# Optimization experiments

Hardware: AMD Instinct MI355X
Metric: run time of the kernel (lower is better)

## Reference

```python
import jax, jax.numpy as jnp
import numpy as np

LORA_RANK = 16
LORA_ALPHA = 32.0
LORA_SCALE = LORA_ALPHA / LORA_RANK
W_BITS = 8
A_BITS = 8


def fake_quant(x, bits):
    """Symmetric per-tensor fake quantization with straight-through estimator."""
    qmax = 2.0 ** (bits - 1) - 1.0
    scale = jnp.maximum(jnp.max(jnp.abs(x)), 1e-8) / qmax
    q = jnp.clip(jnp.round(x / scale), -qmax, qmax) * scale
    return x + jax.lax.stop_gradient(q - x)  # STE


def quant_linear_lora(x, W, b, A, B):
    # x: [..., in], W: [out, in], A: [r, in], B: [out, r]
    xq = fake_quant(x, A_BITS)
    Wq = fake_quant(W, W_BITS)
    base = jnp.einsum('bsi,oi->bso', xq, Wq) + b
    lora = jnp.einsum('bsr,or->bso', jnp.einsum('bsi,ri->bsr', x, A), B)
    return base + LORA_SCALE * lora


def setup_inputs() -> dict:
    key = jax.random.key(0)
    ks = jax.random.split(key, 9)
    n_embd, d_ff, B_, S = 1024, 4096, 4, 2048
    s_in = 1.0 / np.sqrt(n_embd)
    s_ff = 1.0 / np.sqrt(d_ff)
    return {
        'hidden_states': jax.random.normal(ks[0], (B_, S, n_embd), jnp.float32),
        'W_fc': jax.random.normal(ks[1], (d_ff, n_embd), jnp.float32) * s_in,
        'b_fc': jax.random.normal(ks[2], (d_ff,), jnp.float32) * 0.02,
        'A_fc': jax.random.normal(ks[3], (LORA_RANK, n_embd), jnp.float32) * s_in,
        'B_fc': jax.random.normal(ks[4], (d_ff, LORA_RANK), jnp.float32) * 0.01,
        'W_proj': jax.random.normal(ks[5], (n_embd, d_ff), jnp.float32) * s_ff,
        'b_proj': jax.random.normal(ks[6], (n_embd,), jnp.float32) * 0.02,
        'A_proj': jax.random.normal(ks[7], (LORA_RANK, d_ff), jnp.float32) * s_ff,
        'B_proj': jax.random.normal(ks[8], (n_embd, LORA_RANK), jnp.float32) * 0.01,
    }


def reference(hidden_states, W_fc, b_fc, A_fc, B_fc, W_proj, b_proj, A_proj, B_proj):
    h = quant_linear_lora(hidden_states, W_fc, b_fc, A_fc, B_fc)
    h = jax.nn.gelu(h, approximate=False)  # nn.GELU() default = exact erf GELU
    h = quant_linear_lora(h, W_proj, b_proj, A_proj, B_proj)
    return h
```

## Files before the change

kernel.cpp:

```cpp
#include <hip/hip_runtime.h>
#include <stdint.h>

using i32x4 = __attribute__((ext_vector_type(4))) int;
using f32x4 = __attribute__((ext_vector_type(4))) float;
using f16x4 = __attribute__((ext_vector_type(4))) _Float16;

#define M_TOK 8192
#define N_EMB 1024
#define D_FF  4096

__device__ __forceinline__ void async_lds16(void* lds, const void* g) {
  __builtin_amdgcn_global_load_lds(
      (const __attribute__((address_space(1))) void*)g,
      (__attribute__((address_space(3))) void*)lds, 16, 0, 0);
}

__global__ void zero_slots_k(unsigned* s) {
  if (threadIdx.x < 16) s[threadIdx.x] = 0u;
}

__global__ void absmax_k(const float* __restrict__ p, long n, unsigned* __restrict__ slot) {
  long i = ((long)blockIdx.x * blockDim.x + threadIdx.x) * 4;
  long stride = (long)gridDim.x * blockDim.x * 4;
  float m = 0.f;
  for (; i < n; i += stride) {
    float4 v = *(const float4*)(p + i);
    m = fmaxf(m, fmaxf(fmaxf(fabsf(v.x), fabsf(v.y)), fmaxf(fabsf(v.z), fabsf(v.w))));
  }
  for (int o = 32; o; o >>= 1) m = fmaxf(m, __shfl_xor(m, o));
  __shared__ float sm[4];
  if ((threadIdx.x & 63) == 0) sm[threadIdx.x >> 6] = m;
  __syncthreads();
  if (threadIdx.x == 0) {
    m = fmaxf(fmaxf(sm[0], sm[1]), fmaxf(sm[2], sm[3]));
    atomicMax(slot, __float_as_uint(m));
  }
}

__global__ void quant_k(const float* __restrict__ p, int8_t* __restrict__ q, long n,
                        const unsigned* __restrict__ slot) {
  float inv = 127.f / fmaxf(__uint_as_float(*slot), 1e-8f);
  long i = ((long)blockIdx.x * blockDim.x + threadIdx.x) * 4;
  long stride = (long)gridDim.x * blockDim.x * 4;
  for (; i < n; i += stride) {
    float4 v = *(const float4*)(p + i);
    int b0 = (int)fminf(fmaxf(rintf(v.x * inv), -127.f), 127.f);
    int b1 = (int)fminf(fmaxf(rintf(v.y * inv), -127.f), 127.f);
    int b2 = (int)fminf(fmaxf(rintf(v.z * inv), -127.f), 127.f);
    int b3 = (int)fminf(fmaxf(rintf(v.w * inv), -127.f), 127.f);
    int w = (b0 & 0xff) | ((b1 & 0xff) << 8) | ((b2 & 0xff) << 16) | ((b3 & 0xff) << 24);
    *(int*)(q + i) = w;
  }
}

__global__ void prep_bfrag_k(const float* __restrict__ A, _Float16* __restrict__ Bp, int K) {
  int s = blockIdx.x;
  int l = threadIdx.x;
  int r = l & 15, g = l >> 4;
  float4 v = *(const float4*)(A + (long)r * K + s * 16 + g * 4);
  f16x4 h;
  h[0] = (_Float16)v.x; h[1] = (_Float16)v.y; h[2] = (_Float16)v.z; h[3] = (_Float16)v.w;
  *(f16x4*)(Bp + ((long)s * 64 + l) * 4) = h;
}

__global__ __launch_bounds__(512) void lora_quant_k(
    const float* __restrict__ X, const _Float16* __restrict__ Bpre,
    const unsigned* __restrict__ slot, int8_t* __restrict__ Q,
    float* __restrict__ T, int K) {
  int lane = threadIdx.x & 63, wave = threadIdx.x >> 6;
  int row0 = blockIdx.x * 16;
  int r = lane & 15, g = lane >> 4;
  float inv = 127.f / fmaxf(__uint_as_float(*slot), 1e-8f);

  int kPerWave = K >> 3;
  int kbase = wave * kPerWave;
  const float* xrow = X + (long)(row0 + r) * K;
  int8_t* qrow = Q + (long)(row0 + r) * K;

  f32x4 acc = {0.f, 0.f, 0.f, 0.f};
  int nsteps = kPerWave >> 4;
#pragma unroll 4
  for (int s = 0; s < nsteps; s++) {
    int k = kbase + s * 16 + g * 4;
    float4 v = *(const float4*)(xrow + k);
    int b0 = (int)fminf(fmaxf(rintf(v.x * inv), -127.f), 127.f);
    int b1 = (int)fminf(fmaxf(rintf(v.y * inv), -127.f), 127.f);
    int b2 = (int)fminf(fmaxf(rintf(v.z * inv), -127.f), 127.f);
    int b3 = (int)fminf(fmaxf(rintf(v.w * inv), -127.f), 127.f);
    *(int*)(qrow + k) = (b0 & 0xff) | ((b1 & 0xff) << 8) | ((b2 & 0xff) << 16) | ((b3 & 0xff) << 24);
    f16x4 a;
    a[0] = (_Float16)v.x; a[1] = (_Float16)v.y; a[2] = (_Float16)v.z; a[3] = (_Float16)v.w;
    int gs = (kbase + s * 16) >> 4;
    f16x4 b = *(const f16x4*)(Bpre + ((long)gs * 64 + lane) * 4);
    acc = __builtin_amdgcn_mfma_f32_16x16x16f16(a, b, acc, 0, 0, 0);
  }

  __shared__ float part[8][16][17];
#pragma unroll
  for (int j = 0; j < 4; j++) part[wave][g * 4 + j][r] = acc[j];
  __syncthreads();
  int t = threadIdx.x;
  if (t < 256) {
    int m = t >> 4, rr = t & 15;
    float sum = 0.f;
#pragma unroll
    for (int w = 0; w < 8; w++) sum += part[w][m][rr];
    T[(long)(row0 + m) * 16 + rr] = 2.0f * sum;
  }
}

template <bool GELU, int NF>
__global__ __launch_bounds__(512, 2) void gemm8p(
    const int8_t* __restrict__ Aq, const int8_t* __restrict__ Bq,
    int N, int K,
    const unsigned* __restrict__ sa, const unsigned* __restrict__ sb,
    const float* __restrict__ bias,
    const float* __restrict__ T,
    const float* __restrict__ Bl,
    float* __restrict__ C, unsigned* hmax) {
  constexpr int BN = NF * 64;
  constexpr int BBUF = BN * 128;
  __shared__ __align__(16) int8_t lds[65536 + 2 * BBUF];
  int8_t* ldsA = lds;
  int8_t* ldsB = lds + 65536;

  int nwg = gridDim.x * gridDim.y;
  int lid = blockIdx.y * gridDim.x + blockIdx.x;
  int cpx = nwg >> 3;
  int nid = (lid & 7) * cpx + (lid >> 3);
  int bn = (nid % gridDim.x) * BN;
  int bm = (nid / gridDim.x) * 256;

  int t = threadIdx.x;
  int lane = t & 63, wave = t >> 6;
  int wr = wave >> 2, wc = wave & 3;
  int l16 = lane & 15, lq = lane >> 4;

  const int8_t* gA = Aq + (long)bm * K;
  const int8_t* gB = Bq + (long)bn * K;

  int aDst[4], aSrc[4];
#pragma unroll
  for (int i = 0; i < 4; i++) {
    int s = i * 512 + t, row = s >> 3;
    aDst[i] = s * 16;
    aSrc[i] = row * K + (((s & 7) ^ (row & 7)) << 4);
  }
  int bDst[NF], bSrc[NF];
#pragma unroll
  for (int i = 0; i < NF; i++) {
    int s = i * 512 + t, row = s >> 3;
    bDst[i] = s * 16;
    bSrc[i] = row * K + (((s & 7) ^ (row & 7)) << 4);
  }

  int aoff[8], boff[NF];
#pragma unroll
  for (int mf = 0; mf < 8; mf++) {
    int row = wr * 128 + mf * 16 + l16;
    aoff[mf] = row * 128 + ((lq ^ (row & 7)) << 4);
  }
#pragma unroll
  for (int nf = 0; nf < NF; nf++) {
    int row = wc * (NF * 16) + nf * 16 + l16;
    boff[nf] = row * 128 + ((lq ^ (row & 7)) << 4);
  }

  i32x4 acc[8][NF] = {};
  int KT = K >> 7;

#pragma unroll
  for (int i = 0; i < 4; i++) async_lds16(ldsA + aDst[i], gA + aSrc[i]);
#pragma unroll
  for (int i = 0; i < NF; i++) async_lds16(ldsB + bDst[i], gB + bSrc[i]);
#pragma unroll
  for (int i = 0; i < 4; i++) async_lds16(ldsA + 32768 + aDst[i], gA + aSrc[i] + 128);
  asm volatile("s_waitcnt vmcnt(4)" ::: "memory");
  __builtin_amdgcn_s_barrier();
  __builtin_amdgcn_sched_barrier(0);

  for (int kt = 0; kt < KT; ++kt) {
    const int8_t* Ab = ldsA + (kt & 1) * 32768;
    const int8_t* Bb = ldsB + (kt & 1) * BBUF;

    if (kt + 1 < KT) {
      long ko = (long)(kt + 1) * 128;
      int nb = ((kt + 1) & 1) * BBUF;
#pragma unroll
      for (int i = 0; i < NF; i++) async_lds16(ldsB + nb + bDst[i], gB + bSrc[i] + ko);
    }

#pragma unroll
    for (int ks = 0; ks < 2; ks++) {
      int kx = ks << 6;
      i32x4 av[8], bv[NF];
#pragma unroll
      for (int mf = 0; mf < 8; mf++) av[mf] = *(const i32x4*)(Ab + (aoff[mf] ^ kx));
#pragma unroll
      for (int nf = 0; nf < NF; nf++) bv[nf] = *(const i32x4*)(Bb + (boff[nf] ^ kx));
      __builtin_amdgcn_s_setprio(1);
#pragma unroll
      for (int mf = 0; mf < 8; mf++)
#pragma unroll
        for (int nf = 0; nf < NF; nf++)
          acc[mf][nf] = __builtin_amdgcn_mfma_i32_16x16x64_i8(av[mf], bv[nf], acc[mf][nf], 0, 0, 0);
      __builtin_amdgcn_s_setprio(0);
    }

    __builtin_amdgcn_sched_barrier(0);
    __builtin_amdgcn_s_barrier();
    if (kt + 2 < KT) {
      long ko = (long)(kt + 2) * 128;
      int nb = (kt & 1) * 32768;
#pragma unroll
      for (int i = 0; i < 4; i++) async_lds16(ldsA + nb + aDst[i], gA + aSrc[i] + ko);
      asm volatile("s_waitcnt vmcnt(4)" ::: "memory");
      __builtin_amdgcn_s_barrier();
      __builtin_amdgcn_sched_barrier(0);
    } else if (kt + 1 < KT) {
      asm volatile("s_waitcnt vmcnt(0)" ::: "memory");
      __builtin_amdgcn_s_barrier();
      __builtin_amdgcn_sched_barrier(0);
    }
  }

  float s = (fmaxf(__uint_as_float(*sa), 1e-8f) * (1.f / 127.f)) *
            (fmaxf(__uint_as_float(*sb), 1e-8f) * (1.f / 127.f));

  f16x4 af[8], bf[NF];
#pragma unroll
  for (int mf = 0; mf < 8; mf++) {
    int m = bm + wr * 128 + mf * 16 + l16;
    float4 tv = *(const float4*)(T + (long)m * 16 + lq * 4);
    f16x4 v; v[0] = (_Float16)tv.x; v[1] = (_Float16)tv.y; v[2] = (_Float16)tv.z; v[3] = (_Float16)tv.w;
    af[mf] = v;
  }
#pragma unroll
  for (int nf = 0; nf < NF; nf++) {
    int n = bn + wc * (NF * 16) + nf * 16 + l16;
    float4 bv4 = *(const float4*)(Bl + (long)n * 16 + lq * 4);
    f16x4 v; v[0] = (_Float16)bv4.x; v[1] = (_Float16)bv4.y; v[2] = (_Float16)bv4.z; v[3] = (_Float16)bv4.w;
    bf[nf] = v;
  }
  float bias_v[NF];
#pragma unroll
  for (int nf = 0; nf < NF; nf++) bias_v[nf] = bias[bn + wc * (NF * 16) + nf * 16 + l16];

  float lmax = 0.f;
#pragma unroll
  for (int mf = 0; mf < 8; mf++) {
#pragma unroll
    for (int nf = 0; nf < NF; nf++) {
      f32x4 fa = __builtin_amdgcn_mfma_f32_16x16x16f16(af[mf], bf[nf], f32x4{0.f, 0.f, 0.f, 0.f}, 0, 0, 0);
      int n = bn + wc * (NF * 16) + nf * 16 + l16;
#pragma unroll
      for (int j = 0; j < 4; j++) {
        int m = bm + wr * 128 + mf * 16 + lq * 4 + j;
        float v = s * (float)acc[mf][nf][j] + bias_v[nf] + fa[j];
        if constexpr (GELU) {
          v = 0.5f * v * (1.0f + erff(v * 0.70710678118654752f));
          lmax = fmaxf(lmax, fabsf(v));
        }
        C[(long)m * N + n] = v;
      }
    }
  }
  if constexpr (GELU) {
    for (int o = 32; o; o >>= 1) lmax = fmaxf(lmax, __shfl_xor(lmax, o));
    if (lane == 0) atomicMax(hmax, __float_as_uint(lmax));
  }
}

extern "C" void kernel_launch(void* const* d_in, const int* in_sizes, int n_in,
                              void* d_out, int out_size, void* d_ws, size_t ws_size,
                              hipStream_t stream) {
  const float* x   = (const float*)d_in[0];
  const float* Wfc = (const float*)d_in[1];
  const float* bfc = (const float*)d_in[2];
  const float* Afc = (const float*)d_in[3];
  const float* Bfc = (const float*)d_in[4];
  const float* Wpj = (const float*)d_in[5];
  const float* bpj = (const float*)d_in[6];
  const float* Apj = (const float*)d_in[7];
  const float* Bpj = (const float*)d_in[8];
  float* out = (float*)d_out;

  char* ws = (char*)d_ws;
  unsigned* slots = (unsigned*)ws;
  int8_t* qx  = (int8_t*)(ws + 256);
  int8_t* qwf = qx  + (size_t)M_TOK * N_EMB;
  int8_t* qwp = qwf + (size_t)D_FF * N_EMB;
  int8_t* qh  = qwp + (size_t)N_EMB * D_FF;
  float*  t1  = (float*)(qh + (size_t)M_TOK * D_FF);
  float*  t2  = t1  + (size_t)M_TOK * 16;
  _Float16* Bp1 = (_Float16*)(t2 + (size_t)M_TOK * 16);
  _Float16* Bp2 = Bp1 + (size_t)N_EMB * 16;
  float*  h   = (float*)(Bp2 + (size_t)D_FF * 16);

  zero_slots_k<<<1, 64, 0, stream>>>(slots);
  absmax_k<<<1024, 256, 0, stream>>>(x,   (long)M_TOK * N_EMB, slots + 0);
  absmax_k<<<1024, 256, 0, stream>>>(Wfc, (long)D_FF * N_EMB,  slots + 1);
  absmax_k<<<1024, 256, 0, stream>>>(Wpj, (long)N_EMB * D_FF,  slots + 2);

  quant_k<<<2048, 256, 0, stream>>>(Wfc, qwf, (long)D_FF * N_EMB, slots + 1);
  quant_k<<<2048, 256, 0, stream>>>(Wpj, qwp, (long)N_EMB * D_FF, slots + 2);

  prep_bfrag_k<<<N_EMB / 16, 64, 0, stream>>>(Afc, Bp1, N_EMB);
  prep_bfrag_k<<<D_FF / 16, 64, 0, stream>>>(Apj, Bp2, D_FF);

  lora_quant_k<<<M_TOK / 16, 512, 0, stream>>>(x, Bp1, slots + 0, qx, t1, N_EMB);

  gemm8p<true, 4><<<dim3(D_FF / 256, M_TOK / 256), 512, 0, stream>>>(
      qx, qwf, D_FF, N_EMB, slots + 0, slots + 1, bfc, t1, Bfc, h, slots + 3);

  lora_quant_k<<<M_TOK / 16, 512, 0, stream>>>(h, Bp2, slots + 3, qh, t2, D_FF);

  gemm8p<false, 2><<<dim3(N_EMB / 128, M_TOK / 256), 512, 0, stream>>>(
      qh, qwp, N_EMB, D_FF, slots + 3, slots + 2, bpj, t2, Bpj, out, nullptr);
}
```

Baseline: 280.2 us.

## Rework int8 GEMM into templated tile kernel with BK=64 and split MFMA phases

Replaces the int8 GEMM with a templated kernel that uses a K-step of 64 instead of 128, halving LDS per stage and adjusting the swizzle, with both A and B double-buffered and prefetched together. Each K-step is split into two MFMA halves with a barrier between them, and launch bounds move to 4 waves per SIMD for higher occupancy. The second GEMM now uses 128x128 tiles with 256 threads, giving more workgroups. The cost is more loop iterations and barriers, plus a full vmcnt(0) wait each step, which may expose global latency.

```diff
diff --git a/kernel.cpp b/kernel.cpp
--- a/kernel.cpp
+++ b/kernel.cpp
@@ -109,8 +109,8 @@
   }
 }
 
-template <bool GELU, int NF>
-__global__ __launch_bounds__(512, 2) void gemm8p(
+template <bool GELU, int BM, int BN, int THREADS>
+__global__ __launch_bounds__(THREADS, 4) void gemm_tp(
     const int8_t* __restrict__ Aq, const int8_t* __restrict__ Bq,
     int N, int K,
     const unsigned* __restrict__ sa, const unsigned* __restrict__ sb,
@@ -118,144 +118,144 @@
     const float* __restrict__ T,
     const float* __restrict__ Bl,
     float* __restrict__ C, unsigned* hmax) {
-  constexpr int BN = NF * 64;
-  constexpr int BBUF = BN * 128;
-  __shared__ __align__(16) int8_t lds[65536 + 2 * BBUF];
-  int8_t* ldsA = lds;
-  int8_t* ldsB = lds + 65536;
+  constexpr int WM = 2;
+  constexpr int WN = (THREADS / 64) / WM;
+  constexpr int MFR = BM / WM / 16;
+  constexpr int NFR = BN / WN / 16;
+  constexpr int MH = MFR / 2;
+  constexpr int ABYTES = BM * 64;
+  constexpr int BBYTES = BN * 64;
+  constexpr int AL = ABYTES / 16 / THREADS;
+  constexpr int BL = BBYTES / 16 / THREADS;
+  __shared__ __align__(16) int8_t lds[2 * (ABYTES + BBYTES)];
 
   int nwg = gridDim.x * gridDim.y;
   int lid = blockIdx.y * gridDim.x + blockIdx.x;
   int cpx = nwg >> 3;
   int nid = (lid & 7) * cpx + (lid >> 3);
   int bn = (nid % gridDim.x) * BN;
-  int bm = (nid / gridDim.x) * 256;
+  int bm = (nid / gridDim.x) * BM;
 
   int t = threadIdx.x;
   int lane = t & 63, wave = t >> 6;
-  int wr = wave >> 2, wc = wave & 3;
+  int wr = wave / WN, wc = wave % WN;
   int l16 = lane & 15, lq = lane >> 4;
 
-  const int8_t* gA = Aq + (long)bm * K;
-  const int8_t* gB = Bq + (long)bn * K;
-
-  int aDst[4], aSrc[4];
-#pragma unroll
-  for (int i = 0; i < 4; i++) {
-    int s = i * 512 + t, row = s >> 3;
+  int aDst[AL]; const int8_t* srcA[AL];
+#pragma unroll
+  for (int i = 0; i < AL; i++) {
+    int s = i * THREADS + t, row = s >> 2;
+    int key = (row ^ (row >> 2)) & 3;
     aDst[i] = s * 16;
-    aSrc[i] = row * K + (((s & 7) ^ (row & 7)) << 4);
-  }
-  int bDst[NF], bSrc[NF];
-#pragma unroll
-  for (int i = 0; i < NF; i++) {
-    int s = i * 512 + t, row = s >> 3;
+    srcA[i] = Aq + (long)(bm + row) * K + (((s & 3) ^ key) << 4);
+  }
+  int bDst[BL]; const int8_t* srcB[BL];
+#pragma unroll
+  for (int i = 0; i < BL; i++) {
+    int s = i * THREADS + t, row = s >> 2;
+    int key = (row ^ (row >> 2)) & 3;
     bDst[i] = s * 16;
-    bSrc[i] = row * K + (((s & 7) ^ (row & 7)) << 4);
-  }
-
-  int aoff[8], boff[NF];
-#pragma unroll
-  for (int mf = 0; mf < 8; mf++) {
-    int row = wr * 128 + mf * 16 + l16;
-    aoff[mf] = row * 128 + ((lq ^ (row & 7)) << 4);
-  }
-#pragma unroll
-  for (int nf = 0; nf < NF; nf++) {
-    int row = wc * (NF * 16) + nf * 16 + l16;
-    boff[nf] = row * 128 + ((lq ^ (row & 7)) << 4);
-  }
-
-  i32x4 acc[8][NF] = {};
-  int KT = K >> 7;
-
-#pragma unroll
-  for (int i = 0; i < 4; i++) async_lds16(ldsA + aDst[i], gA + aSrc[i]);
-#pragma unroll
-  for (int i = 0; i < NF; i++) async_lds16(ldsB + bDst[i], gB + bSrc[i]);
-#pragma unroll
-  for (int i = 0; i < 4; i++) async_lds16(ldsA + 32768 + aDst[i], gA + aSrc[i] + 128);
-  asm volatile("s_waitcnt vmcnt(4)" ::: "memory");
-  __builtin_amdgcn_s_barrier();
-  __builtin_amdgcn_sched_barrier(0);
+    srcB[i] = Bq + (long)(bn + row) * K + (((s & 3) ^ key) << 4);
+  }
+
+  int aoff[MFR], boff[NFR];
+#pragma unroll
+  for (int mf = 0; mf < MFR; mf++) {
+    int row = wr * (BM / WM) + mf * 16 + l16;
+    aoff[mf] = row * 64 + ((lq ^ ((row ^ (row >> 2)) & 3)) << 4);
+  }
+#pragma unroll
+  for (int nf = 0; nf < NFR; nf++) {
+    int row = wc * (BN / WN) + nf * 16 + l16;
+    boff[nf] = row * 64 + ((lq ^ ((row ^ (row >> 2)) & 3)) << 4);
+  }
+
+  i32x4 acc[MFR][NFR] = {};
+  int KT = K >> 6;
+
+#pragma unroll
+  for (int i = 0; i < AL; i++) async_lds16(lds + aDst[i], srcA[i]);
+#pragma unroll
+  for (int i = 0; i < BL; i++) async_lds16(lds + ABYTES + bDst[i], srcB[i]);
 
   for (int kt = 0; kt < KT; ++kt) {
-    const int8_t* Ab = ldsA + (kt & 1) * 32768;
-    const int8_t* Bb = ldsB + (kt & 1) * BBUF;
+    const int8_t* base = lds + (kt & 1) * (ABYTES + BBYTES);
+
+    asm volatile("s_waitcnt vmcnt(0)" ::: "memory");
+    __builtin_amdgcn_s_barrier();
+
+    i32x4 av[MH], bv[NFR];
+#pragma unroll
+    for (int j = 0; j < MH; j++) av[j] = *(const i32x4*)(base + aoff[j]);
+#pragma unroll
+    for (int nf = 0; nf < NFR; nf++) bv[nf] = *(const i32x4*)(base + ABYTES + boff[nf]);
 
     if (kt + 1 < KT) {
-      long ko = (long)(kt + 1) * 128;
-      int nb = ((kt + 1) & 1) * BBUF;
-#pragma unroll
-      for (int i = 0; i < NF; i++) async_lds16(ldsB + nb + bDst[i], gB + bSrc[i] + ko);
+      long ko = (long)(kt + 1) * 64;
+      int8_t* nb = lds + ((kt + 1) & 1) * (ABYTES + BBYTES);
+#pragma unroll
+      for (int i = 0; i < AL; i++) async_lds16(nb + aDst[i], srcA[i] + ko);
+#pragma unroll
+      for (int i = 0; i < BL; i++) async_lds16(nb + ABYTES + bDst[i], srcB[i] + ko);
     }
 
-#pragma unroll
-    for (int ks = 0; ks < 2; ks++) {
-      int kx = ks << 6;
-      i32x4 av[8], bv[NF];
-#pragma unroll
-      for (int mf = 0; mf < 8; mf++) av[mf] = *(const i32x4*)(Ab + (aoff[mf] ^ kx));
-#pragma unroll
-      for (int nf = 0; nf < NF; nf++) bv[nf] = *(const i32x4*)(Bb + (boff[nf] ^ kx));
-      __builtin_amdgcn_s_setprio(1);
-#pragma unroll
-      for (int mf = 0; mf < 8; mf++)
-#pragma unroll
-        for (int nf = 0; nf < NF; nf++)
-          acc[mf][nf] = __builtin_amdgcn_mfma_i32_16x16x64_i8(av[mf], bv[nf], acc[mf][nf], 0, 0, 0);
-      __builtin_amdgcn_s_setprio(0);
-    }
-
+    asm volatile("s_waitcnt lgkmcnt(0)" ::: "memory");
     __builtin_amdgcn_sched_barrier(0);
+    __builtin_amdgcn_s_setprio(1);
+#pragma unroll
+    for (int j = 0; j < MH; j++)
+#pragma unroll
+      for (int nf = 0; nf < NFR; nf++)
+        acc[j][nf] = __builtin_amdgcn_mfma_i32_16x16x64_i8(av[j], bv[nf], acc[j][nf], 0, 0, 0);
+    __builtin_amdgcn_s_setprio(0);
     __builtin_amdgcn_s_barrier();
-    if (kt + 2 < KT) {
-      long ko = (long)(kt + 2) * 128;
-      int nb = (kt & 1) * 32768;
-#pragma unroll
-      for (int i = 0; i < 4; i++) async_lds16(ldsA + nb + aDst[i], gA + aSrc[i] + ko);
-      asm volatile("s_waitcnt vmcnt(4)" ::: "memory");
-      __builtin_amdgcn_s_barrier();
-      __builtin_amdgcn_sched_barrier(0);
-    } else if (kt + 1 < KT) {
-      asm volatile("s_waitcnt vmcnt(0)" ::: "memory");
-      __builtin_amdgcn_s_barrier();
-      __builtin_amdgcn_sched_barrier(0);
-    }
+
+    i32x4 av2[MH];
+#pragma unroll
+    for (int j = 0; j < MH; j++) av2[j] = *(const i32x4*)(base + aoff[MH + j]);
+    asm volatile("s_waitcnt lgkmcnt(0)" ::: "memory");
+    __builtin_amdgcn_sched_barrier(0);
+    __builtin_amdgcn_s_setprio(1);
+#pragma unroll
+    for (int j = 0; j < MH; j++)
+#pragma unroll
+      for (int nf = 0; nf < NFR; nf++)
+        acc[MH + j][nf] = __builtin_amdgcn_mfma_i32_16x16x64_i8(av2[j], bv[nf], acc[MH + j][nf], 0, 0, 0);
+    __builtin_amdgcn_s_setprio(0);
   }
 
   float s = (fmaxf(__uint_as_float(*sa), 1e-8f) * (1.f / 127.f)) *
             (fmaxf(__uint_as_float(*sb), 1e-8f) * (1.f / 127.f));
 
-  f16x4 af[8], bf[NF];
-#pragma unroll
-  for (int mf = 0; mf < 8; mf++) {
-    int m = bm + wr * 128 + mf * 16 + l16;
+  f16x4 af[MFR], bf[NFR];
+#pragma unroll
+  for (int mf = 0; mf < MFR; mf++) {
+    int m = bm + wr * (BM / WM) + mf * 16 + l16;
     float4 tv = *(const float4*)(T + (long)m * 16 + lq * 4);
     f16x4 v; v[0] = (_Float16)tv.x; v[1] = (_Float16)tv.y; v[2] = (_Float16)tv.z; v[3] = (_Float16)tv.w;
     af[mf] = v;
   }
 #pragma unroll
-  for (int nf = 0; nf < NF; nf++) {
-    int n = bn + wc * (NF * 16) + nf * 16 + l16;
+  for (int nf = 0; nf < NFR; nf++) {
+    int n = bn + wc * (BN / WN) + nf * 16 + l16;
     float4 bv4 = *(const float4*)(Bl + (long)n * 16 + lq * 4);
     f16x4 v; v[0] = (_Float16)bv4.x; v[1] = (_Float16)bv4.y; v[2] = (_Float16)bv4.z; v[3] = (_Float16)bv4.w;
     bf[nf] = v;
   }
-  float bias_v[NF];
-#pragma unroll
-  for (int nf = 0; nf < NF; nf++) bias_v[nf] = bias[bn + wc * (NF * 16) + nf * 16 + l16];
+  float bias_v[NFR];
+#pragma unroll
+  for (int nf = 0; nf < NFR; nf++) bias_v[nf] = bias[bn + wc * (BN / WN) + nf * 16 + l16];
 
   float lmax = 0.f;
 #pragma unroll
-  for (int mf = 0; mf < 8; mf++) {
-#pragma unroll
-    for (int nf = 0; nf < NF; nf++) {
+  for (int mf = 0; mf < MFR; mf++) {
+#pragma unroll
+    for (int nf = 0; nf < NFR; nf++) {
       f32x4 fa = __builtin_amdgcn_mfma_f32_16x16x16f16(af[mf], bf[nf], f32x4{0.f, 0.f, 0.f, 0.f}, 0, 0, 0);
-      int n = bn + wc * (NF * 16) + nf * 16 + l16;
+      int n = bn + wc * (BN / WN) + nf * 16 + l16;
 #pragma unroll
       for (int j = 0; j < 4; j++) {
-        int m = bm + wr * 128 + mf * 16 + lq * 4 + j;
+        int m = bm + wr * (BM / WM) + mf * 16 + lq * 4 + j;
         float v = s * (float)acc[mf][nf][j] + bias_v[nf] + fa[j];
         if constexpr (GELU) {
           v = 0.5f * v * (1.0f + erff(v * 0.70710678118654752f));
@@ -310,11 +310,11 @@
 
   lora_quant_k<<<M_TOK / 16, 512, 0, stream>>>(x, Bp1, slots + 0, qx, t1, N_EMB);
 
-  gemm8p<true, 4><<<dim3(D_FF / 256, M_TOK / 256), 512, 0, stream>>>(
+  gemm_tp<true, 256, 256, 512><<<dim3(D_FF / 256, M_TOK / 256), 512, 0, stream>>>(
       qx, qwf, D_FF, N_EMB, slots + 0, slots + 1, bfc, t1, Bfc, h, slots + 3);
 
   lora_quant_k<<<M_TOK / 16, 512, 0, stream>>>(h, Bp2, slots + 3, qh, t2, D_FF);
 
-  gemm8p<false, 2><<<dim3(N_EMB / 128, M_TOK / 256), 512, 0, stream>>>(
+  gemm_tp<false, 128, 128, 256><<<dim3(N_EMB / 128, M_TOK / 128), 256, 0, stream>>>(
       qh, qwp, N_EMB, D_FF, slots + 3, slots + 2, bpj, t2, Bpj, out, nullptr);
 }
```

Measured after the change: 518.5 us. 85.0% more time.

## Switch int8 GEMMs from 16x16x64 to 32x32x32 MFMA tiles

Applied to the files above, without the earlier changes.

Replaces the 16x16x64 int8 MFMA inner loop with 32x32x32 int8 MFMA, so each wave holds 4xNFR 32x32 accumulator tiles and the LDS fragment offsets are re-derived for 32-row fragments. The LoRA epilogue also moves to a 32x32x16 f16 MFMA, with the output row mapping changed to match. Larger MFMA tiles need fewer LDS fragment reads per FLOP and fewer instruction issues. The launch-bounds occupancy hint of 2 is dropped and the source offsets are widened to long.

```diff
diff --git a/kernel.cpp b/kernel.cpp
--- a/kernel.cpp
+++ b/kernel.cpp
@@ -1,9 +1,12 @@
 #include <hip/hip_runtime.h>
 #include <stdint.h>
 
-using i32x4 = __attribute__((ext_vector_type(4))) int;
-using f32x4 = __attribute__((ext_vector_type(4))) float;
-using f16x4 = __attribute__((ext_vector_type(4))) _Float16;
+using i32x4  = __attribute__((ext_vector_type(4))) int;
+using i32x16 = __attribute__((ext_vector_type(16))) int;
+using f32x4  = __attribute__((ext_vector_type(4))) float;
+using f32x16 = __attribute__((ext_vector_type(16))) float;
+using f16x4  = __attribute__((ext_vector_type(4))) _Float16;
+using f16x8  = __attribute__((ext_vector_type(8))) _Float16;
 
 #define M_TOK 8192
 #define N_EMB 1024
@@ -109,8 +112,8 @@
   }
 }
 
-template <bool GELU, int NF>
-__global__ __launch_bounds__(512, 2) void gemm8p(
+template <bool GELU, int NFR>
+__global__ __launch_bounds__(512) void gemm32(
     const int8_t* __restrict__ Aq, const int8_t* __restrict__ Bq,
     int N, int K,
     const unsigned* __restrict__ sa, const unsigned* __restrict__ sb,
@@ -118,11 +121,13 @@
     const float* __restrict__ T,
     const float* __restrict__ Bl,
     float* __restrict__ C, unsigned* hmax) {
-  constexpr int BN = NF * 64;
-  constexpr int BBUF = BN * 128;
-  __shared__ __align__(16) int8_t lds[65536 + 2 * BBUF];
+  constexpr int BN = NFR * 128;
+  constexpr int ABYTES = 32768;
+  constexpr int BBYTES = BN * 128;
+  constexpr int BL = BBYTES / 16 / 512;
+  __shared__ __align__(16) int8_t lds[2 * ABYTES + 2 * BBYTES];
   int8_t* ldsA = lds;
-  int8_t* ldsB = lds + 65536;
+  int8_t* ldsB = lds + 2 * ABYTES;
 
   int nwg = gridDim.x * gridDim.y;
   int lid = blockIdx.y * gridDim.x + blockIdx.x;
@@ -134,76 +139,76 @@
   int t = threadIdx.x;
   int lane = t & 63, wave = t >> 6;
   int wr = wave >> 2, wc = wave & 3;
-  int l16 = lane & 15, lq = lane >> 4;
+  int l31 = lane & 31, l5 = lane >> 5;
 
   const int8_t* gA = Aq + (long)bm * K;
   const int8_t* gB = Bq + (long)bn * K;
 
-  int aDst[4], aSrc[4];
+  int aDst[4]; long aSrc[4];
 #pragma unroll
   for (int i = 0; i < 4; i++) {
     int s = i * 512 + t, row = s >> 3;
     aDst[i] = s * 16;
-    aSrc[i] = row * K + (((s & 7) ^ (row & 7)) << 4);
-  }
-  int bDst[NF], bSrc[NF];
-#pragma unroll
-  for (int i = 0; i < NF; i++) {
+    aSrc[i] = (long)row * K + (((s & 7) ^ (row & 7)) << 4);
+  }
+  int bDst[BL]; long bSrc[BL];
+#pragma unroll
+  for (int i = 0; i < BL; i++) {
     int s = i * 512 + t, row = s >> 3;
     bDst[i] = s * 16;
-    bSrc[i] = row * K + (((s & 7) ^ (row & 7)) << 4);
-  }
-
-  int aoff[8], boff[NF];
-#pragma unroll
-  for (int mf = 0; mf < 8; mf++) {
-    int row = wr * 128 + mf * 16 + l16;
-    aoff[mf] = row * 128 + ((lq ^ (row & 7)) << 4);
-  }
-#pragma unroll
-  for (int nf = 0; nf < NF; nf++) {
-    int row = wc * (NF * 16) + nf * 16 + l16;
-    boff[nf] = row * 128 + ((lq ^ (row & 7)) << 4);
-  }
-
-  i32x4 acc[8][NF] = {};
+    bSrc[i] = (long)row * K + (((s & 7) ^ (row & 7)) << 4);
+  }
+
+  int aoff[4], boff[NFR];
+#pragma unroll
+  for (int mf = 0; mf < 4; mf++) {
+    int row = wr * 128 + mf * 32 + l31;
+    aoff[mf] = row * 128 + ((l5 ^ (row & 7)) << 4);
+  }
+#pragma unroll
+  for (int nf = 0; nf < NFR; nf++) {
+    int row = wc * (NFR * 32) + nf * 32 + l31;
+    boff[nf] = row * 128 + ((l5 ^ (row & 7)) << 4);
+  }
+
+  i32x16 acc[4][NFR] = {};
   int KT = K >> 7;
 
 #pragma unroll
   for (int i = 0; i < 4; i++) async_lds16(ldsA + aDst[i], gA + aSrc[i]);
 #pragma unroll
-  for (int i = 0; i < NF; i++) async_lds16(ldsB + bDst[i], gB + bSrc[i]);
-#pragma unroll
-  for (int i = 0; i < 4; i++) async_lds16(ldsA + 32768 + aDst[i], gA + aSrc[i] + 128);
+  for (int i = 0; i < BL; i++) async_lds16(ldsB + bDst[i], gB + bSrc[i]);
+#pragma unroll
+  for (int i = 0; i < 4; i++) async_lds16(ldsA + ABYTES + aDst[i], gA + aSrc[i] + 128);
   asm volatile("s_waitcnt vmcnt(4)" ::: "memory");
   __builtin_amdgcn_s_barrier();
   __builtin_amdgcn_sched_barrier(0);
 
   for (int kt = 0; kt < KT; ++kt) {
-    const int8_t* Ab = ldsA + (kt & 1) * 32768;
-    const int8_t* Bb = ldsB + (kt & 1) * BBUF;
+    const int8_t* Ab = ldsA + (kt & 1) * ABYTES;
+    const int8_t* Bb = ldsB + (kt & 1) * BBYTES;
 
     if (kt + 1 < KT) {
       long ko = (long)(kt + 1) * 128;
-      int nb = ((kt + 1) & 1) * BBUF;
-#pragma unroll
-      for (int i = 0; i < NF; i++) async_lds16(ldsB + nb + bDst[i], gB + bSrc[i] + ko);
+      int nb = ((kt + 1) & 1) * BBYTES;
+#pragma unroll
+      for (int i = 0; i < BL; i++) async_lds16(ldsB + nb + bDst[i], gB + bSrc[i] + ko);
     }
 
 #pragma unroll
-    for (int ks = 0; ks < 2; ks++) {
-      int kx = ks << 6;
-      i32x4 av[8], bv[NF];
-#pragma unroll
-      for (int mf = 0; mf < 8; mf++) av[mf] = *(const i32x4*)(Ab + (aoff[mf] ^ kx));
-#pragma unroll
-      for (int nf = 0; nf < NF; nf++) bv[nf] = *(const i32x4*)(Bb + (boff[nf] ^ kx));
+    for (int ks = 0; ks < 4; ks++) {
+      int kx = ks << 5;
+      i32x4 av[4], bv[NFR];
+#pragma unroll
+      for (int mf = 0; mf < 4; mf++) av[mf] = *(const i32x4*)(Ab + (aoff[mf] ^ kx));
+#pragma unroll
+      for (int nf = 0; nf < NFR; nf++) bv[nf] = *(const i32x4*)(Bb + (boff[nf] ^ kx));
       __builtin_amdgcn_s_setprio(1);
 #pragma unroll
-      for (int mf = 0; mf < 8; mf++)
-#pragma unroll
-        for (int nf = 0; nf < NF; nf++)
-          acc[mf][nf] = __builtin_amdgcn_mfma_i32_16x16x64_i8(av[mf], bv[nf], acc[mf][nf], 0, 0, 0);
+      for (int mf = 0; mf < 4; mf++)
+#pragma unroll
+        for (int nf = 0; nf < NFR; nf++)
+          acc[mf][nf] = __builtin_amdgcn_mfma_i32_32x32x32_i8(av[mf], bv[nf], acc[mf][nf], 0, 0, 0);
       __builtin_amdgcn_s_setprio(0);
     }
 
@@ -211,7 +216,7 @@
     __builtin_amdgcn_s_barrier();
     if (kt + 2 < KT) {
       long ko = (long)(kt + 2) * 128;
-      int nb = (kt & 1) * 32768;
+      int nb = (kt & 1) * ABYTES;
 #pragma unroll
       for (int i = 0; i < 4; i++) async_lds16(ldsA + nb + aDst[i], gA + aSrc[i] + ko);
       asm volatile("s_waitcnt vmcnt(4)" ::: "memory");
@@ -227,36 +232,43 @@
   float s = (fmaxf(__uint_as_float(*sa), 1e-8f) * (1.f / 127.f)) *
             (fmaxf(__uint_as_float(*sb), 1e-8f) * (1.f / 127.f));
 
-  f16x4 af[8], bf[NF];
-#pragma unroll
-  for (int mf = 0; mf < 8; mf++) {
-    int m = bm + wr * 128 + mf * 16 + l16;
-    float4 tv = *(const float4*)(T + (long)m * 16 + lq * 4);
-    f16x4 v; v[0] = (_Float16)tv.x; v[1] = (_Float16)tv.y; v[2] = (_Float16)tv.z; v[3] = (_Float16)tv.w;
-    af[mf] = v;
-  }
-#pragma unroll
-  for (int nf = 0; nf < NF; nf++) {
-    int n = bn + wc * (NF * 16) + nf * 16 + l16;
-    float4 bv4 = *(const float4*)(Bl + (long)n * 16 + lq * 4);
-    f16x4 v; v[0] = (_Float16)bv4.x; v[1] = (_Float16)bv4.y; v[2] = (_Float16)bv4.z; v[3] = (_Float16)bv4.w;
-    bf[nf] = v;
-  }
-  float bias_v[NF];
-#pragma unroll
-  for (int nf = 0; nf < NF; nf++) bias_v[nf] = bias[bn + wc * (NF * 16) + nf * 16 + l16];
+  f16x8 tf[4];
+#pragma unroll
+  for (int mf = 0; mf < 4; mf++) {
+    int m = bm + wr * 128 + mf * 32 + l31;
+    float4 t0 = *(const float4*)(T + (long)m * 16 + l5 * 8);
+    float4 t1 = *(const float4*)(T + (long)m * 16 + l5 * 8 + 4);
+    f16x8 v;
+    v[0] = (_Float16)t0.x; v[1] = (_Float16)t0.y; v[2] = (_Float16)t0.z; v[3] = (_Float16)t0.w;
+    v[4] = (_Float16)t1.x; v[5] = (_Float16)t1.y; v[6] = (_Float16)t1.z; v[7] = (_Float16)t1.w;
+    tf[mf] = v;
+  }
+  f16x8 bfr[NFR];
+  float bias_v[NFR];
+#pragma unroll
+  for (int nf = 0; nf < NFR; nf++) {
+    int n = bn + wc * (NFR * 32) + nf * 32 + l31;
+    float4 b0 = *(const float4*)(Bl + (long)n * 16 + l5 * 8);
+    float4 b1 = *(const float4*)(Bl + (long)n * 16 + l5 * 8 + 4);
+    f16x8 v;
+    v[0] = (_Float16)b0.x; v[1] = (_Float16)b0.y; v[2] = (_Float16)b0.z; v[3] = (_Float16)b0.w;
+    v[4] = (_Float16)b1.x; v[5] = (_Float16)b1.y; v[6] = (_Float16)b1.z; v[7] = (_Float16)b1.w;
+    bfr[nf] = v;
+    bias_v[nf] = bias[n];
+  }
 
   float lmax = 0.f;
 #pragma unroll
-  for (int mf = 0; mf < 8; mf++) {
-#pragma unroll
-    for (int nf = 0; nf < NF; nf++) {
-      f32x4 fa = __builtin_amdgcn_mfma_f32_16x16x16f16(af[mf], bf[nf], f32x4{0.f, 0.f, 0.f, 0.f}, 0, 0, 0);
-      int n = bn + wc * (NF * 16) + nf * 16 + l16;
-#pragma unroll
-      for (int j = 0; j < 4; j++) {
-        int m = bm + wr * 128 + mf * 16 + lq * 4 + j;
-        float v = s * (float)acc[mf][nf][j] + bias_v[nf] + fa[j];
+  for (int mf = 0; mf < 4; mf++) {
+#pragma unroll
+    for (int nf = 0; nf < NFR; nf++) {
+      f32x16 fa = __builtin_amdgcn_mfma_f32_32x32x16_f16(tf[mf], bfr[nf], (f32x16){}, 0, 0, 0);
+      int n = bn + wc * (NFR * 32) + nf * 32 + l31;
+#pragma unroll
+      for (int reg = 0; reg < 16; reg++) {
+        int row = (reg & 3) + 8 * (reg >> 2) + 4 * l5;
+        int m = bm + wr * 128 + mf * 32 + row;
+        float v = s * (float)acc[mf][nf][reg] + bias_v[nf] + fa[reg];
         if constexpr (GELU) {
           v = 0.5f * v * (1.0f + erff(v * 0.70710678118654752f));
           lmax = fmaxf(lmax, fabsf(v));
@@ -310,11 +322,11 @@
 
   lora_quant_k<<<M_TOK / 16, 512, 0, stream>>>(x, Bp1, slots + 0, qx, t1, N_EMB);
 
-  gemm8p<true, 4><<<dim3(D_FF / 256, M_TOK / 256), 512, 0, stream>>>(
+  gemm32<true, 2><<<dim3(D_FF / 256, M_TOK / 256), 512, 0, stream>>>(
       qx, qwf, D_FF, N_EMB, slots + 0, slots + 1, bfc, t1, Bfc, h, slots + 3);
 
   lora_quant_k<<<M_TOK / 16, 512, 0, stream>>>(h, Bp2, slots + 3, qh, t2, D_FF);
 
-  gemm8p<false, 2><<<dim3(N_EMB / 128, M_TOK / 256), 512, 0, stream>>>(
+  gemm32<false, 1><<<dim3(N_EMB / 128, M_TOK / 256), 512, 0, stream>>>(
       qh, qwp, N_EMB, D_FF, slots + 3, slots + 2, bpj, t2, Bpj, out, nullptr);
 }
```

After: 286.1 us. 1.02x slower.
